# Kernel optimization log

Measured on AMD Instinct MI355X. Metric: run time of the kernel, lower is better.

The kernel has to match this reference:

```python
import jax, jax.numpy as jnp
import numpy as np

N_NODES = 100000
N_HEDGES = 100000
N_INC = 3200000
N_LINKS = 262144


def setup_inputs() -> dict:
    key = jax.random.key(0)
    ks = jax.random.split(key, 8)
    X = jax.random.normal(ks[0], (N_NODES, 128), dtype=jnp.float32)
    inc_v = jax.random.randint(ks[1], (N_INC,), 0, N_NODES)
    inc_e = jnp.sort(jax.random.randint(ks[2], (N_INC,), 0, N_HEDGES))
    link = jax.random.randint(ks[3], (N_LINKS, 2), 0, N_NODES)
    init = lambda k, shape, fan_in: jax.random.normal(k, shape, dtype=jnp.float32) / np.float32(np.sqrt(fan_in))
    W1 = init(ks[4], (128, 256), 128); b1 = jnp.zeros((256,), jnp.float32)
    W2 = init(ks[5], (256, 128), 256); b2 = jnp.zeros((128,), jnp.float32)
    fcW = init(ks[6], (128, 1), 128); fcb = jnp.zeros((1,), jnp.float32)
    return dict(X=X, W1=W1, b1=b1, W2=W2, b2=b2, fcW=fcW, fcb=fcb,
                inc_v=inc_v, inc_e=inc_e, link=link)


def _smooth(X, inc_v, inc_e, dv_isqrt, de_inv):
    # D_v^{-1/2} H D_e^{-1} H^T D_v^{-1/2} X  (unit hyperedge weights)
    Xs = X * dv_isqrt[:, None]                                              # [N, C]
    Ye = jax.ops.segment_sum(Xs[inc_v], inc_e, num_segments=N_HEDGES)       # [E, C]
    Ye = Ye * de_inv[:, None]
    Xo = jax.ops.segment_sum(Ye[inc_e], inc_v, num_segments=N_NODES)        # [N, C]
    return Xo * dv_isqrt[:, None]


def reference(X, W1, b1, W2, b2, fcW, fcb, inc_v, inc_e, link):
    ones = jnp.ones(inc_v.shape, dtype=jnp.float32)
    dv = jax.ops.segment_sum(ones, inc_v, num_segments=N_NODES)
    de = jax.ops.segment_sum(ones, inc_e, num_segments=N_HEDGES)
    dv_isqrt = jnp.where(dv > 0, jax.lax.rsqrt(jnp.maximum(dv, 1.0)), 0.0)
    de_inv = jnp.where(de > 0, 1.0 / jnp.maximum(de, 1.0), 0.0)
    # conv1: linear -> smoothing -> relu (dropout is identity in eval mode);
    # encode() applies an extra .relu() which is idempotent after ReLU.
    h = jax.nn.relu(_smooth(X @ W1 + b1, inc_v, inc_e, dv_isqrt, de_inv))
    # conv2
    z = jax.nn.relu(_smooth(h @ W2 + b2, inc_v, inc_e, dv_isqrt, de_inv))
    # link pooling: mean of endpoint embeddings, then Linear + Sigmoid
    pooled = z[link].mean(axis=1)                                           # [L, C]
    return jax.nn.sigmoid(pooled @ fcW + fcb)                               # [L, 1]
```

## Files before the change

kernel.cpp:

```cpp
#include <hip/hip_runtime.h>
#include <math.h>

#define N_NODES  100000
#define N_HEDGES 100000
#define N_INC    3200000
#define N_LINKS  262144

typedef unsigned short u16;

constexpr int C1 = 128;
constexpr int NBKT = 782;
constexpr int RSV_STRIDE = 16;
constexpr int BCAP = 8192;
constexpr int P1_NB = 400;
constexpr int P1_CHUNK = 8000;

__device__ __forceinline__ float4 b4f(ushort4 u) {
    float4 f;
    f.x = __uint_as_float(((unsigned)u.x) << 16);
    f.y = __uint_as_float(((unsigned)u.y) << 16);
    f.z = __uint_as_float(((unsigned)u.z) << 16);
    f.w = __uint_as_float(((unsigned)u.w) << 16);
    return f;
}
__device__ __forceinline__ u16 f2b(float f) {
    unsigned u = __float_as_uint(f);
    u += 0x7FFFu + ((u >> 16) & 1u);
    return (u16)(u >> 16);
}


__global__ void k_init2(int* hoff, int* hend, int* rsv) {
    int i = blockIdx.x * blockDim.x + threadIdx.x;
    if (i < N_HEDGES) { hoff[i] = 0; hend[i] = 0; }
    if (i < NBKT * RSV_STRIDE) rsv[i] = 0;
}

__global__ void k_boundary(const int* __restrict__ inc_e, int* __restrict__ hoff,
                           int* __restrict__ hend) {
    int i = blockIdx.x * blockDim.x + threadIdx.x;
    if (i >= N_INC) return;
    int e = inc_e[i];
    if (i == 0 || inc_e[i - 1] != e) hoff[e] = i;
    if (i == N_INC - 1 || inc_e[i + 1] != e) hend[e] = i + 1;
}

__global__ void k_transform_e(const int* __restrict__ hoff, const int* __restrict__ hend,
                              int* __restrict__ de_cnt, float* __restrict__ de_inv) {
    int e = blockIdx.x * blockDim.x + threadIdx.x;
    if (e >= N_HEDGES) return;
    int d = hend[e] - hoff[e];
    de_cnt[e] = d;
    de_inv[e] = (d > 0) ? 1.0f / (float)d : 0.0f;
}

__global__ __launch_bounds__(256) void k_phase1(const int* __restrict__ inc_v,
                                                const int* __restrict__ inc_e,
                                                int* __restrict__ rsv,
                                                uint2* __restrict__ pairs) {
    __shared__ int hist[NBKT];
    __shared__ int base[NBKT];
    const int t = threadIdx.x;
    const int start = blockIdx.x * P1_CHUNK;
    for (int b = t; b < NBKT; b += 256) hist[b] = 0;
    __syncthreads();
    for (int i = start + t; i < start + P1_CHUNK; i += 256)
        atomicAdd(&hist[inc_v[i] >> 7], 1);
    __syncthreads();
    for (int b = t; b < NBKT; b += 256) {
        int c = hist[b];
        base[b] = (c > 0) ? atomicAdd(&rsv[b * RSV_STRIDE], c) : 0;
        hist[b] = 0;
    }
    __syncthreads();
    for (int i = start + t; i < start + P1_CHUNK; i += 256) {
        int v = inc_v[i];
        int e = inc_e[i];
        int b = v >> 7;
        int r = base[b] + atomicAdd(&hist[b], 1);
        if (r < BCAP)
            pairs[(size_t)b * BCAP + r] = make_uint2((unsigned)v, (unsigned)e);
    }
}

__global__ void k_scan_buckets(const int* __restrict__ rsv, int* __restrict__ bucket_base) {
    __shared__ int s[1024];
    int t = threadIdx.x;
    int own = (t < NBKT) ? rsv[t * RSV_STRIDE] : 0;
    s[t] = own;
    __syncthreads();
    for (int off = 1; off < 1024; off <<= 1) {
        int v = (t >= off) ? s[t - off] : 0;
        __syncthreads();
        s[t] += v;
        __syncthreads();
    }
    if (t < NBKT) bucket_base[t] = s[t] - own;
}

__global__ __launch_bounds__(256) void k_phase2(const int* __restrict__ rsv,
                                                const int* __restrict__ bucket_base,
                                                const uint2* __restrict__ pairs,
                                                int* __restrict__ csr_e,
                                                int* __restrict__ dv_cnt,
                                                float* __restrict__ dv_isqrt,
                                                int* __restrict__ noff) {
    __shared__ int cnt[128];
    __shared__ int pfx[128];
    __shared__ int curs[128];
    const int t = threadIdx.x;
    const int b = blockIdx.x;
    int sz = rsv[b * RSV_STRIDE];
    if (sz > BCAP) sz = BCAP;
    const int gbase = bucket_base[b];
    const uint2* mp = pairs + (size_t)b * BCAP;
    if (t < 128) cnt[t] = 0;
    __syncthreads();
    for (int i = t; i < sz; i += 256)
        atomicAdd(&cnt[mp[i].x & 127], 1);
    __syncthreads();
    if (t < 128) pfx[t] = cnt[t];
    __syncthreads();
    for (int off = 1; off < 128; off <<= 1) {
        int v = (t < 128 && t >= off) ? pfx[t - off] : 0;
        __syncthreads();
        if (t < 128) pfx[t] += v;
        __syncthreads();
    }
    if (t < 128) {
        int excl = pfx[t] - cnt[t];
        curs[t] = excl;
        int v = (b << 7) + t;
        if (v < N_NODES) {
            int c = cnt[t];
            dv_cnt[v] = c;
            dv_isqrt[v] = (c > 0) ? 1.0f / sqrtf((float)c) : 0.0f;
            noff[v] = gbase + excl;
        }
    }
    __syncthreads();
    for (int i = t; i < sz; i += 256) {
        uint2 p = mp[i];
        int r = atomicAdd(&curs[p.x & 127], 1);
        csr_e[gbase + r] = (int)p.y;
    }
}


__global__ void k_x2b(const float* __restrict__ X, u16* __restrict__ Xb) {
    int i = blockIdx.x * blockDim.x + threadIdx.x;
    if (i >= N_NODES * C1 / 4) return;
    float4 x = reinterpret_cast<const float4*>(X)[i];
    reinterpret_cast<ushort4*>(Xb)[i] = make_ushort4(f2b(x.x), f2b(x.y), f2b(x.z), f2b(x.w));
}


template <bool WS>
__global__ void k_gather_edges_b(const int* __restrict__ hoff, const int* __restrict__ de_cnt,
                                 const int* __restrict__ inc_v, const u16* __restrict__ in,
                                 const float* __restrict__ dv_isqrt, const float* __restrict__ de_inv,
                                 u16* __restrict__ out, float* __restrict__ se) {
    int gw = (blockIdx.x * blockDim.x + threadIdx.x) >> 6;
    int lane = threadIdx.x & 63;
    if (gw >= N_HEDGES) return;
    int half = lane >> 5;
    int l = lane & 31;
    int st = hoff[gw], n = de_cnt[gw];
    float4 acc = {0.f, 0.f, 0.f, 0.f};
    float ws = 0.f;
    int j = half;
    for (; j + 14 < n; j += 16) {
        int v[8]; float w[8]; ushort4 r[8];
#pragma unroll
        for (int q = 0; q < 8; ++q) v[q] = inc_v[st + j + 2 * q];
#pragma unroll
        for (int q = 0; q < 8; ++q) w[q] = dv_isqrt[v[q]];
#pragma unroll
        for (int q = 0; q < 8; ++q)
            r[q] = *reinterpret_cast<const ushort4*>(in + (size_t)v[q] * C1 + l * 4);
#pragma unroll
        for (int q = 0; q < 8; ++q) {
            if (WS) ws += w[q];
            float4 x = b4f(r[q]);
            acc.x = fmaf(w[q], x.x, acc.x); acc.y = fmaf(w[q], x.y, acc.y);
            acc.z = fmaf(w[q], x.z, acc.z); acc.w = fmaf(w[q], x.w, acc.w);
        }
    }
    for (; j < n; j += 2) {
        int v = inc_v[st + j];
        float w = dv_isqrt[v];
        float4 x = b4f(*reinterpret_cast<const ushort4*>(in + (size_t)v * C1 + l * 4));
        if (WS) ws += w;
        acc.x = fmaf(w, x.x, acc.x); acc.y = fmaf(w, x.y, acc.y);
        acc.z = fmaf(w, x.z, acc.z); acc.w = fmaf(w, x.w, acc.w);
    }
    acc.x += __shfl_xor(acc.x, 32);
    acc.y += __shfl_xor(acc.y, 32);
    acc.z += __shfl_xor(acc.z, 32);
    acc.w += __shfl_xor(acc.w, 32);
    if (WS) ws += __shfl_xor(ws, 32);
    if (half == 0) {
        float sc = de_inv[gw];
        *reinterpret_cast<ushort4*>(out + (size_t)gw * C1 + l * 4) =
            make_ushort4(f2b(acc.x * sc), f2b(acc.y * sc), f2b(acc.z * sc), f2b(acc.w * sc));
        if (WS && l == 0) se[gw] = ws * sc;
    }
}

template <bool SV>
__global__ void k_gather_nodes_b(const int* __restrict__ noff, const int* __restrict__ dv_cnt,
                                 const int* __restrict__ csr_e, const u16* __restrict__ in,
                                 const float* __restrict__ dv_isqrt, float* __restrict__ out,
                                 const float* __restrict__ se, float* __restrict__ svec) {
    int gw = (blockIdx.x * blockDim.x + threadIdx.x) >> 6;
    int lane = threadIdx.x & 63;
    if (gw >= N_NODES) return;
    int half = lane >> 5;
    int l = lane & 31;
    int st = noff[gw], n = dv_cnt[gw];
    float4 acc = {0.f, 0.f, 0.f, 0.f};
    float sv = 0.f;
    int j = half;
    for (; j + 14 < n; j += 16) {
        int e[8]; ushort4 r[8];
#pragma unroll
        for (int q = 0; q < 8; ++q) e[q] = csr_e[st + j + 2 * q];
#pragma unroll
        for (int q = 0; q < 8; ++q)
            r[q] = *reinterpret_cast<const ushort4*>(in + (size_t)e[q] * C1 + l * 4);
#pragma unroll
        for (int q = 0; q < 8; ++q) {
            if (SV) sv += se[e[q]];
            float4 y = b4f(r[q]);
            acc.x += y.x; acc.y += y.y; acc.z += y.z; acc.w += y.w;
        }
    }
    for (; j < n; j += 2) {
        int e = csr_e[st + j];
        float4 y = b4f(*reinterpret_cast<const ushort4*>(in + (size_t)e * C1 + l * 4));
        if (SV) sv += se[e];
        acc.x += y.x; acc.y += y.y; acc.z += y.z; acc.w += y.w;
    }
    acc.x += __shfl_xor(acc.x, 32);
    acc.y += __shfl_xor(acc.y, 32);
    acc.z += __shfl_xor(acc.z, 32);
    acc.w += __shfl_xor(acc.w, 32);
    if (SV) sv += __shfl_xor(sv, 32);
    if (half == 0) {
        float sc = dv_isqrt[gw];
        float4 o = {acc.x * sc, acc.y * sc, acc.z * sc, acc.w * sc};
        *reinterpret_cast<float4*>(out + (size_t)gw * C1 + l * 4) = o;
        if (SV && l == 0) svec[gw] = sv * sc;
    }
}

__global__ void k_gather_nodes_fc_b(const int* __restrict__ noff, const int* __restrict__ dv_cnt,
                                    const int* __restrict__ csr_e, const u16* __restrict__ in,
                                    const float* __restrict__ dv_isqrt, const float* __restrict__ fcW,
                                    float* __restrict__ t) {
    int gw = (blockIdx.x * blockDim.x + threadIdx.x) >> 6;
    int lane = threadIdx.x & 63;
    if (gw >= N_NODES) return;
    int half = lane >> 5;
    int l = lane & 31;
    int st = noff[gw], n = dv_cnt[gw];
    float4 acc = {0.f, 0.f, 0.f, 0.f};
    int j = half;
    for (; j + 14 < n; j += 16) {
        int e[8]; ushort4 r[8];
#pragma unroll
        for (int q = 0; q < 8; ++q) e[q] = csr_e[st + j + 2 * q];
#pragma unroll
        for (int q = 0; q < 8; ++q)
            r[q] = *reinterpret_cast<const ushort4*>(in + (size_t)e[q] * C1 + l * 4);
#pragma unroll
        for (int q = 0; q < 8; ++q) {
            float4 y = b4f(r[q]);
            acc.x += y.x; acc.y += y.y; acc.z += y.z; acc.w += y.w;
        }
    }
    for (; j < n; j += 2) {
        int e = csr_e[st + j];
        float4 y = b4f(*reinterpret_cast<const ushort4*>(in + (size_t)e * C1 + l * 4));
        acc.x += y.x; acc.y += y.y; acc.z += y.z; acc.w += y.w;
    }
    acc.x += __shfl_xor(acc.x, 32);
    acc.y += __shfl_xor(acc.y, 32);
    acc.z += __shfl_xor(acc.z, 32);
    acc.w += __shfl_xor(acc.w, 32);
    float sc = dv_isqrt[gw];
    float4 w = *reinterpret_cast<const float4*>(fcW + l * 4);
    float p = fmaxf(acc.x * sc, 0.f) * w.x + fmaxf(acc.y * sc, 0.f) * w.y +
              fmaxf(acc.z * sc, 0.f) * w.z + fmaxf(acc.w * sc, 0.f) * w.w;
#pragma unroll
    for (int off = 16; off > 0; off >>= 1) p += __shfl_xor(p, off);
    if (lane == 0) t[gw] = p;
}

template <int K, int EPI>
__global__ __launch_bounds__(256, 2) void k_gemm(const float* __restrict__ A,
                                                 const float* __restrict__ B,
                                                 const float* __restrict__ bias,
                                                 const float* __restrict__ svec,
                                                 float* __restrict__ C, int M, int N) {
    __shared__ float As[16][132];
    __shared__ float Bs[16][132];
    const int tid = threadIdx.x;
    const int bm = blockIdx.y * 128;
    const int bn = blockIdx.x * 128;
    const int rm = (tid >> 4) * 4;
    const int cn = (tid & 15) * 4;
    float acc[8][8] = {};

    const int arow = tid >> 2;
    const int akc  = (tid & 3) * 4;
    const int brow = tid >> 5;
    const int bcol = (tid & 31) * 4;

    for (int kk = 0; kk < K; kk += 16) {
#pragma unroll
        for (int h = 0; h < 2; ++h) {
            int row = bm + arow + h * 64;
            float4 a = {0.f, 0.f, 0.f, 0.f};
            if (row < M) a = *reinterpret_cast<const float4*>(A + (size_t)row * K + kk + akc);
            As[akc + 0][arow + h * 64] = a.x;
            As[akc + 1][arow + h * 64] = a.y;
            As[akc + 2][arow + h * 64] = a.z;
            As[akc + 3][arow + h * 64] = a.w;
        }
#pragma unroll
        for (int h = 0; h < 2; ++h) {
            int kr = brow + h * 8;
            *reinterpret_cast<float4*>(&Bs[kr][bcol]) =
                *reinterpret_cast<const float4*>(B + (size_t)(kk + kr) * N + bn + bcol);
        }
        __syncthreads();
#pragma unroll
        for (int k = 0; k < 16; ++k) {
            float4 a0 = *reinterpret_cast<const float4*>(&As[k][rm]);
            float4 a1 = *reinterpret_cast<const float4*>(&As[k][64 + rm]);
            float4 b0 = *reinterpret_cast<const float4*>(&Bs[k][cn]);
            float4 b1 = *reinterpret_cast<const float4*>(&Bs[k][64 + cn]);
            float av[8] = {a0.x, a0.y, a0.z, a0.w, a1.x, a1.y, a1.z, a1.w};
            float bv[8] = {b0.x, b0.y, b0.z, b0.w, b1.x, b1.y, b1.z, b1.w};
#pragma unroll
            for (int i = 0; i < 8; ++i)
#pragma unroll
                for (int j = 0; j < 8; ++j)
                    acc[i][j] = fmaf(av[i], bv[j], acc[i][j]);
        }
        __syncthreads();
    }

    const float4 bv0 = *reinterpret_cast<const float4*>(bias + bn + cn);
    const float4 bv1 = *reinterpret_cast<const float4*>(bias + bn + 64 + cn);
    const float bb0[4] = {bv0.x, bv0.y, bv0.z, bv0.w};
    const float bb1[4] = {bv1.x, bv1.y, bv1.z, bv1.w};
#pragma unroll
    for (int i = 0; i < 8; ++i) {
        int row = bm + ((i < 4) ? (rm + i) : (64 + rm + i - 4));
        if (row >= M) continue;
        float s = (EPI == 1) ? svec[row] : 0.f;
        float v0[4], v1[4];
#pragma unroll
        for (int j = 0; j < 4; ++j) {
            if (EPI == 1) {
                v0[j] = fmaxf(fmaf(s, bb0[j], acc[i][j]), 0.f);
                v1[j] = fmaxf(fmaf(s, bb1[j], acc[i][j + 4]), 0.f);
            } else {
                v0[j] = acc[i][j] + bb0[j];
                v1[j] = acc[i][j + 4] + bb1[j];
            }
        }
        if (EPI == 3) {
            u16* Cb = (u16*)C;
            *reinterpret_cast<ushort4*>(Cb + (size_t)row * N + bn + cn) =
                make_ushort4(f2b(v0[0]), f2b(v0[1]), f2b(v0[2]), f2b(v0[3]));
            *reinterpret_cast<ushort4*>(Cb + (size_t)row * N + bn + 64 + cn) =
                make_ushort4(f2b(v1[0]), f2b(v1[1]), f2b(v1[2]), f2b(v1[3]));
        } else {
            float4 o0 = {v0[0], v0[1], v0[2], v0[3]};
            float4 o1 = {v1[0], v1[1], v1[2], v1[3]};
            *reinterpret_cast<float4*>(C + (size_t)row * N + bn + cn) = o0;
            *reinterpret_cast<float4*>(C + (size_t)row * N + bn + 64 + cn) = o1;
        }
    }
}


__global__ void k_link(const int* __restrict__ link, const float* __restrict__ t,
                       const float* __restrict__ fcb, float* __restrict__ out) {
    int l = blockIdx.x * blockDim.x + threadIdx.x;
    if (l >= N_LINKS) return;
    int a = link[2 * l], b = link[2 * l + 1];
    float x = 0.5f * (t[a] + t[b]) + fcb[0];
    out[l] = 1.f / (1.f + expf(-x));
}


extern "C" void kernel_launch(void* const* d_in, const int* in_sizes, int n_in,
                              void* d_out, int out_size, void* d_ws, size_t ws_size,
                              hipStream_t stream) {
    const float* X    = (const float*)d_in[0];
    const float* W1   = (const float*)d_in[1];
    const float* b1   = (const float*)d_in[2];
    const float* W2   = (const float*)d_in[3];
    const float* b2   = (const float*)d_in[4];
    const float* fcW  = (const float*)d_in[5];
    const float* fcb  = (const float*)d_in[6];
    const int* inc_v  = (const int*)d_in[7];
    const int* inc_e  = (const int*)d_in[8];
    const int* link   = (const int*)d_in[9];
    float* out = (float*)d_out;

    size_t off = 0;
    auto carve = [&](size_t nbytes) -> void* {
        void* p = (char*)d_ws + off;
        off += (nbytes + 255) & ~(size_t)255;
        return p;
    };
    int* hoff    = (int*)carve((size_t)N_HEDGES * 4);
    int* hend    = (int*)carve((size_t)N_HEDGES * 4);
    int* de_cnt  = (int*)carve((size_t)N_HEDGES * 4);
    int* dv_cnt  = (int*)carve((size_t)N_NODES * 4);
    int* noff    = (int*)carve((size_t)N_NODES * 4);
    int* rsv     = (int*)carve((size_t)NBKT * RSV_STRIDE * 4);
    int* bucket_base = (int*)carve((size_t)NBKT * 4);
    float* dv_isqrt = (float*)carve((size_t)N_NODES * 4);
    float* de_inv   = (float*)carve((size_t)N_HEDGES * 4);
    float* se    = (float*)carve((size_t)N_HEDGES * 4);
    float* svec  = (float*)carve((size_t)N_NODES * 4);
    float* tvec  = (float*)carve((size_t)N_NODES * 4);
    int* csr_e   = (int*)carve((size_t)N_INC * 4);
    float* R0    = (float*)carve((size_t)N_NODES * 256 * 4);
    float* Xs    = (float*)carve((size_t)N_NODES * C1 * 4);
    uint2* pairs = (uint2*)R0;
    u16*   Yeb   = (u16*)R0;
    float* H     = R0;
    u16*   Xb    = (u16*)Xs;
    u16*   T2b   = (u16*)Xs;

    if (off > ws_size) return;

    k_init2<<<(N_HEDGES + 255) / 256, 256, 0, stream>>>(hoff, hend, rsv);
    k_boundary<<<N_INC / 256, 256, 0, stream>>>(inc_e, hoff, hend);
    k_transform_e<<<(N_HEDGES + 255) / 256, 256, 0, stream>>>(hoff, hend, de_cnt, de_inv);
    k_phase1<<<P1_NB, 256, 0, stream>>>(inc_v, inc_e, rsv, pairs);
    k_scan_buckets<<<1, 1024, 0, stream>>>(rsv, bucket_base);
    k_phase2<<<NBKT, 256, 0, stream>>>(rsv, bucket_base, pairs, csr_e, dv_cnt, dv_isqrt, noff);

    k_x2b<<<(N_NODES * C1 / 4 + 255) / 256, 256, 0, stream>>>(X, Xb);

    k_gather_edges_b<true><<<25000, 256, 0, stream>>>(hoff, de_cnt, inc_v, Xb, dv_isqrt, de_inv, Yeb, se);
    k_gather_nodes_b<true><<<25000, 256, 0, stream>>>(noff, dv_cnt, csr_e, Yeb, dv_isqrt, Xs, se, svec);
    k_gemm<128, 1><<<dim3(2, (N_NODES + 127) / 128), 256, 0, stream>>>(Xs, W1, b1, svec, H, N_NODES, 256);

    k_gemm<256, 3><<<dim3(1, (N_NODES + 127) / 128), 256, 0, stream>>>(H, W2, b2, nullptr, (float*)T2b, N_NODES, 128);
    k_gather_edges_b<false><<<25000, 256, 0, stream>>>(hoff, de_cnt, inc_v, T2b, dv_isqrt, de_inv, Yeb, nullptr);
    k_gather_nodes_fc_b<<<25000, 256, 0, stream>>>(noff, dv_cnt, csr_e, Yeb, dv_isqrt, fcW, tvec);

    k_link<<<N_LINKS / 256, 256, 0, stream>>>(link, tvec, fcb, out);
}
```

Measured before the change: 880.6 us.

## Replace FP32 SIMT GEMMs with split-bf16 MFMA GEMMs

Replaces the shared-memory FP32 FMA GEMMs with MFMA bf16 16x16x32 kernels. They use a hi/lo bf16 split (three MFMAs per tile) to keep near-FP32 accuracy. The node gather and the first GEMM now write hi/lo bf16 pairs instead of fp32, and weights are pre-split and transposed by a small kernel. This aims to move the dense work onto matrix cores and cut intermediate bandwidth. In exchange it triples the MFMA count, reads operands straight from global memory without LDS reuse, and writes output with scattered 2-byte stores.

```diff
diff --git a/kernel.cpp b/kernel.cpp
--- a/kernel.cpp
+++ b/kernel.cpp
@@ -15,12 +15,13 @@
 constexpr int P1_NB = 400;
 constexpr int P1_CHUNK = 8000;
 
+typedef __attribute__((ext_vector_type(8))) short short8;
+typedef __attribute__((ext_vector_type(4))) float f32x4;
+
+__device__ __forceinline__ float b2f1(u16 u) { return __uint_as_float(((unsigned)u) << 16); }
 __device__ __forceinline__ float4 b4f(ushort4 u) {
     float4 f;
-    f.x = __uint_as_float(((unsigned)u.x) << 16);
-    f.y = __uint_as_float(((unsigned)u.y) << 16);
-    f.z = __uint_as_float(((unsigned)u.z) << 16);
-    f.w = __uint_as_float(((unsigned)u.w) << 16);
+    f.x = b2f1(u.x); f.y = b2f1(u.y); f.z = b2f1(u.z); f.w = b2f1(u.w);
     return f;
 }
 __device__ __forceinline__ u16 f2b(float f) {
@@ -154,6 +155,17 @@
     reinterpret_cast<ushort4*>(Xb)[i] = make_ushort4(f2b(x.x), f2b(x.y), f2b(x.z), f2b(x.w));
 }
 
+__global__ void k_wsplit(const float* __restrict__ W, u16* __restrict__ Thi,
+                         u16* __restrict__ Tlo, int K, int N) {
+    int i = blockIdx.x * blockDim.x + threadIdx.x;
+    if (i >= K * N) return;
+    int n = i / K, k = i - n * K;
+    float w = W[(size_t)k * N + n];
+    u16 h = f2b(w);
+    Thi[(size_t)n * K + k] = h;
+    Tlo[(size_t)n * K + k] = f2b(w - b2f1(h));
+}
+
 
 template <bool WS>
 __global__ void k_gather_edges_b(const int* __restrict__ hoff, const int* __restrict__ de_cnt,
@@ -207,11 +219,11 @@
     }
 }
 
-template <bool SV>
 __global__ void k_gather_nodes_b(const int* __restrict__ noff, const int* __restrict__ dv_cnt,
                                  const int* __restrict__ csr_e, const u16* __restrict__ in,
-                                 const float* __restrict__ dv_isqrt, float* __restrict__ out,
-                                 const float* __restrict__ se, float* __restrict__ svec) {
+                                 const float* __restrict__ dv_isqrt, u16* __restrict__ out_hi,
+                                 u16* __restrict__ out_lo, const float* __restrict__ se,
+                                 float* __restrict__ svec) {
     int gw = (blockIdx.x * blockDim.x + threadIdx.x) >> 6;
     int lane = threadIdx.x & 63;
     if (gw >= N_NODES) return;
@@ -230,7 +242,7 @@
             r[q] = *reinterpret_cast<const ushort4*>(in + (size_t)e[q] * C1 + l * 4);
 #pragma unroll
         for (int q = 0; q < 8; ++q) {
-            if (SV) sv += se[e[q]];
+            sv += se[e[q]];
             float4 y = b4f(r[q]);
             acc.x += y.x; acc.y += y.y; acc.z += y.z; acc.w += y.w;
         }
@@ -238,19 +250,23 @@
     for (; j < n; j += 2) {
         int e = csr_e[st + j];
         float4 y = b4f(*reinterpret_cast<const ushort4*>(in + (size_t)e * C1 + l * 4));
-        if (SV) sv += se[e];
+        sv += se[e];
         acc.x += y.x; acc.y += y.y; acc.z += y.z; acc.w += y.w;
     }
     acc.x += __shfl_xor(acc.x, 32);
     acc.y += __shfl_xor(acc.y, 32);
     acc.z += __shfl_xor(acc.z, 32);
     acc.w += __shfl_xor(acc.w, 32);
-    if (SV) sv += __shfl_xor(sv, 32);
+    sv += __shfl_xor(sv, 32);
     if (half == 0) {
         float sc = dv_isqrt[gw];
         float4 o = {acc.x * sc, acc.y * sc, acc.z * sc, acc.w * sc};
-        *reinterpret_cast<float4*>(out + (size_t)gw * C1 + l * 4) = o;
-        if (SV && l == 0) svec[gw] = sv * sc;
+        ushort4 hi = make_ushort4(f2b(o.x), f2b(o.y), f2b(o.z), f2b(o.w));
+        ushort4 lo = make_ushort4(f2b(o.x - b2f1(hi.x)), f2b(o.y - b2f1(hi.y)),
+                                  f2b(o.z - b2f1(hi.z)), f2b(o.w - b2f1(hi.w)));
+        *reinterpret_cast<ushort4*>(out_hi + (size_t)gw * C1 + l * 4) = hi;
+        *reinterpret_cast<ushort4*>(out_lo + (size_t)gw * C1 + l * 4) = lo;
+        if (l == 0) svec[gw] = sv * sc;
     }
 }
 
@@ -297,92 +313,61 @@
     if (lane == 0) t[gw] = p;
 }
 
-template <int K, int EPI>
-__global__ __launch_bounds__(256, 2) void k_gemm(const float* __restrict__ A,
-                                                 const float* __restrict__ B,
-                                                 const float* __restrict__ bias,
-                                                 const float* __restrict__ svec,
-                                                 float* __restrict__ C, int M, int N) {
-    __shared__ float As[16][132];
-    __shared__ float Bs[16][132];
+template <int K, int NTW, int EPI>
+__global__ __launch_bounds__(256) void k_gemm_mfma(
+        const u16* __restrict__ Ahi, const u16* __restrict__ Alo,
+        const u16* __restrict__ BThi, const u16* __restrict__ BTlo,
+        const float* __restrict__ bias, const float* __restrict__ svec,
+        u16* __restrict__ outHi, u16* __restrict__ outLo, int N) {
     const int tid = threadIdx.x;
-    const int bm = blockIdx.y * 128;
-    const int bn = blockIdx.x * 128;
-    const int rm = (tid >> 4) * 4;
-    const int cn = (tid & 15) * 4;
-    float acc[8][8] = {};
-
-    const int arow = tid >> 2;
-    const int akc  = (tid & 3) * 4;
-    const int brow = tid >> 5;
-    const int bcol = (tid & 31) * 4;
-
-    for (int kk = 0; kk < K; kk += 16) {
-#pragma unroll
-        for (int h = 0; h < 2; ++h) {
-            int row = bm + arow + h * 64;
-            float4 a = {0.f, 0.f, 0.f, 0.f};
-            if (row < M) a = *reinterpret_cast<const float4*>(A + (size_t)row * K + kk + akc);
-            As[akc + 0][arow + h * 64] = a.x;
-            As[akc + 1][arow + h * 64] = a.y;
-            As[akc + 2][arow + h * 64] = a.z;
-            As[akc + 3][arow + h * 64] = a.w;
-        }
-#pragma unroll
-        for (int h = 0; h < 2; ++h) {
-            int kr = brow + h * 8;
-            *reinterpret_cast<float4*>(&Bs[kr][bcol]) =
-                *reinterpret_cast<const float4*>(B + (size_t)(kk + kr) * N + bn + bcol);
-        }
-        __syncthreads();
-#pragma unroll
-        for (int k = 0; k < 16; ++k) {
-            float4 a0 = *reinterpret_cast<const float4*>(&As[k][rm]);
-            float4 a1 = *reinterpret_cast<const float4*>(&As[k][64 + rm]);
-            float4 b0 = *reinterpret_cast<const float4*>(&Bs[k][cn]);
-            float4 b1 = *reinterpret_cast<const float4*>(&Bs[k][64 + cn]);
-            float av[8] = {a0.x, a0.y, a0.z, a0.w, a1.x, a1.y, a1.z, a1.w};
-            float bv[8] = {b0.x, b0.y, b0.z, b0.w, b1.x, b1.y, b1.z, b1.w};
-#pragma unroll
-            for (int i = 0; i < 8; ++i)
-#pragma unroll
-                for (int j = 0; j < 8; ++j)
-                    acc[i][j] = fmaf(av[i], bv[j], acc[i][j]);
-        }
-        __syncthreads();
-    }
-
-    const float4 bv0 = *reinterpret_cast<const float4*>(bias + bn + cn);
-    const float4 bv1 = *reinterpret_cast<const float4*>(bias + bn + 64 + cn);
-    const float bb0[4] = {bv0.x, bv0.y, bv0.z, bv0.w};
-    const float bb1[4] = {bv1.x, bv1.y, bv1.z, bv1.w};
-#pragma unroll
-    for (int i = 0; i < 8; ++i) {
-        int row = bm + ((i < 4) ? (rm + i) : (64 + rm + i - 4));
-        if (row >= M) continue;
-        float s = (EPI == 1) ? svec[row] : 0.f;
-        float v0[4], v1[4];
-#pragma unroll
-        for (int j = 0; j < 4; ++j) {
+    const int wave = tid >> 6, lane = tid & 63;
+    const int bm = blockIdx.x * 16;
+    const int rr = lane & 15;
+    const int kg = lane >> 4;
+    const int bn = wave * (NTW * 16);
+
+    f32x4 acc[NTW];
+#pragma unroll
+    for (int t = 0; t < NTW; ++t) acc[t] = {0.f, 0.f, 0.f, 0.f};
+
+    const u16* aph = Ahi + (size_t)(bm + rr) * K + kg * 8;
+    const u16* apl = Alo + (size_t)(bm + rr) * K + kg * 8;
+
+    for (int ks = 0; ks < K; ks += 32) {
+        short8 ah = *reinterpret_cast<const short8*>(aph + ks);
+        short8 al = *reinterpret_cast<const short8*>(apl + ks);
+#pragma unroll
+        for (int t = 0; t < NTW; ++t) {
+            size_t boff = (size_t)(bn + t * 16 + rr) * K + ks + kg * 8;
+            short8 bh = *reinterpret_cast<const short8*>(BThi + boff);
+            short8 bl = *reinterpret_cast<const short8*>(BTlo + boff);
+            acc[t] = __builtin_amdgcn_mfma_f32_16x16x32_bf16(ah, bh, acc[t], 0, 0, 0);
+            acc[t] = __builtin_amdgcn_mfma_f32_16x16x32_bf16(ah, bl, acc[t], 0, 0, 0);
+            acc[t] = __builtin_amdgcn_mfma_f32_16x16x32_bf16(al, bh, acc[t], 0, 0, 0);
+        }
+    }
+
+    float sv[4];
+    if (EPI == 1) {
+#pragma unroll
+        for (int r = 0; r < 4; ++r) sv[r] = svec[bm + kg * 4 + r];
+    }
+#pragma unroll
+    for (int t = 0; t < NTW; ++t) {
+        int col = bn + t * 16 + rr;
+        float bc = bias[col];
+#pragma unroll
+        for (int r = 0; r < 4; ++r) {
+            int row = bm + kg * 4 + r;
+            float v = acc[t][r];
             if (EPI == 1) {
-                v0[j] = fmaxf(fmaf(s, bb0[j], acc[i][j]), 0.f);
-                v1[j] = fmaxf(fmaf(s, bb1[j], acc[i][j + 4]), 0.f);
+                v = fmaxf(fmaf(sv[r], bc, v), 0.f);
+                u16 h = f2b(v);
+                outHi[(size_t)row * N + col] = h;
+                outLo[(size_t)row * N + col] = f2b(v - b2f1(h));
             } else {
-                v0[j] = acc[i][j] + bb0[j];
-                v1[j] = acc[i][j + 4] + bb1[j];
+                outHi[(size_t)row * N + col] = f2b(v + bc);
             }
-        }
-        if (EPI == 3) {
-            u16* Cb = (u16*)C;
-            *reinterpret_cast<ushort4*>(Cb + (size_t)row * N + bn + cn) =
-                make_ushort4(f2b(v0[0]), f2b(v0[1]), f2b(v0[2]), f2b(v0[3]));
-            *reinterpret_cast<ushort4*>(Cb + (size_t)row * N + bn + 64 + cn) =
-                make_ushort4(f2b(v1[0]), f2b(v1[1]), f2b(v1[2]), f2b(v1[3]));
-        } else {
-            float4 o0 = {v0[0], v0[1], v0[2], v0[3]};
-            float4 o1 = {v1[0], v1[1], v1[2], v1[3]};
-            *reinterpret_cast<float4*>(C + (size_t)row * N + bn + cn) = o0;
-            *reinterpret_cast<float4*>(C + (size_t)row * N + bn + 64 + cn) = o1;
         }
     }
 }
@@ -432,13 +417,20 @@
     float* svec  = (float*)carve((size_t)N_NODES * 4);
     float* tvec  = (float*)carve((size_t)N_NODES * 4);
     int* csr_e   = (int*)carve((size_t)N_INC * 4);
+    u16* w1th    = (u16*)carve((size_t)256 * 128 * 2);
+    u16* w1tl    = (u16*)carve((size_t)256 * 128 * 2);
+    u16* w2th    = (u16*)carve((size_t)128 * 256 * 2);
+    u16* w2tl    = (u16*)carve((size_t)128 * 256 * 2);
     float* R0    = (float*)carve((size_t)N_NODES * 256 * 4);
-    float* Xs    = (float*)carve((size_t)N_NODES * C1 * 4);
+    float* XsR   = (float*)carve((size_t)N_NODES * C1 * 4);
     uint2* pairs = (uint2*)R0;
     u16*   Yeb   = (u16*)R0;
-    float* H     = R0;
-    u16*   Xb    = (u16*)Xs;
-    u16*   T2b   = (u16*)Xs;
+    u16*   H_hi  = (u16*)R0;
+    u16*   H_lo  = (u16*)R0 + (size_t)N_NODES * 256;
+    u16*   Xb    = (u16*)XsR;
+    u16*   Xs_hi = (u16*)XsR;
+    u16*   Xs_lo = (u16*)XsR + (size_t)N_NODES * C1;
+    u16*   T2b   = (u16*)XsR;
 
     if (off > ws_size) return;
 
@@ -450,12 +442,14 @@
     k_phase2<<<NBKT, 256, 0, stream>>>(rsv, bucket_base, pairs, csr_e, dv_cnt, dv_isqrt, noff);
 
     k_x2b<<<(N_NODES * C1 / 4 + 255) / 256, 256, 0, stream>>>(X, Xb);
+    k_wsplit<<<(128 * 256 + 255) / 256, 256, 0, stream>>>(W1, w1th, w1tl, 128, 256);
+    k_wsplit<<<(256 * 128 + 255) / 256, 256, 0, stream>>>(W2, w2th, w2tl, 256, 128);
 
     k_gather_edges_b<true><<<25000, 256, 0, stream>>>(hoff, de_cnt, inc_v, Xb, dv_isqrt, de_inv, Yeb, se);
-    k_gather_nodes_b<true><<<25000, 256, 0, stream>>>(noff, dv_cnt, csr_e, Yeb, dv_isqrt, Xs, se, svec);
-    k_gemm<128, 1><<<dim3(2, (N_NODES + 127) / 128), 256, 0, stream>>>(Xs, W1, b1, svec, H, N_NODES, 256);
-
-    k_gemm<256, 3><<<dim3(1, (N_NODES + 127) / 128), 256, 0, stream>>>(H, W2, b2, nullptr, (float*)T2b, N_NODES, 128);
+    k_gather_nodes_b<<<25000, 256, 0, stream>>>(noff, dv_cnt, csr_e, Yeb, dv_isqrt, Xs_hi, Xs_lo, se, svec);
+    k_gemm_mfma<128, 4, 1><<<N_NODES / 16, 256, 0, stream>>>(Xs_hi, Xs_lo, w1th, w1tl, b1, svec, H_hi, H_lo, 256);
+
+    k_gemm_mfma<256, 2, 3><<<N_NODES / 16, 256, 0, stream>>>(H_hi, H_lo, w2th, w2tl, b2, nullptr, T2b, nullptr, 128);
     k_gather_edges_b<false><<<25000, 256, 0, stream>>>(hoff, de_cnt, inc_v, T2b, dv_isqrt, de_inv, Yeb, nullptr);
     k_gather_nodes_fc_b<<<25000, 256, 0, stream>>>(noff, dv_cnt, csr_e, Yeb, dv_isqrt, fcW, tvec);
 
```

New measurement: 940.3 us. 6.8% more time.
